# Optimization experiments

Measured on AMD Instinct MI355X. Metric: run time of the kernel, lower is better.

The kernel has to match this reference:

```python
import math
import jax, jax.numpy as jnp
import numpy as np

N = 20000
E = 640000
H = 256          # hidden_channels
HEADS = 8
HD = H // HEADS  # head_dim = 32
RBF = 64
CUT = 5.0
EPS = 1e-5


def setup_inputs() -> dict:
    key = jax.random.key(0)
    ks = jax.random.split(key, 24)
    g = lambda k, shape, scale: (jax.random.normal(k, shape, dtype=jnp.float32) * scale)
    inp = {
        "x": jax.random.normal(ks[0], (N, H), dtype=jnp.float32),
        "vec": jax.random.normal(ks[1], (N, 3, H), dtype=jnp.float32),
        "edge_index": jax.random.randint(ks[2], (2, E), 0, N),
        "r_ij": jax.random.uniform(ks[3], (E,), dtype=jnp.float32) * CUT,
        "f_ij": jax.random.normal(ks[4], (E, RBF), dtype=jnp.float32),
        "d_ij": jax.random.normal(ks[5], (E, 3), dtype=jnp.float32),
        # parameters (weights stored as [in, out], applied as x @ W + b)
        "ln_w": jnp.ones((H,), jnp.float32),
        "ln_b": jnp.zeros((H,), jnp.float32),
        "Wq": g(ks[6], (H, H), 1.0 / math.sqrt(H)),
        "bq": jnp.zeros((H,), jnp.float32),
        "Wk": g(ks[7], (H, H), 1.0 / math.sqrt(H)),
        "bk": jnp.zeros((H,), jnp.float32),
        "Wv": g(ks[8], (H, 3 * H), 1.0 / math.sqrt(H)),
        "bv": jnp.zeros((3 * H,), jnp.float32),
        "Wo": g(ks[9], (H, 3 * H), 1.0 / math.sqrt(H)),
        "bo": jnp.zeros((3 * H,), jnp.float32),
        "Wvec": g(ks[10], (H, 3 * H), 1.0 / math.sqrt(H)),  # no bias
        "Wdk": g(ks[11], (RBF, H), 1.0 / math.sqrt(RBF)),
        "bdk": jnp.zeros((H,), jnp.float32),
        "Wdv": g(ks[12], (RBF, 3 * H), 1.0 / math.sqrt(RBF)),
        "bdv": jnp.zeros((3 * H,), jnp.float32),
    }
    return inp


def reference(x, vec, edge_index, r_ij, f_ij, d_ij,
              ln_w, ln_b, Wq, bq, Wk, bk, Wv, bv, Wo, bo,
              Wvec, Wdk, bdk, Wdv, bdv):
    silu = jax.nn.silu
    n = x.shape[0]

    # LayerNorm over hidden dim
    mu = x.mean(-1, keepdims=True)
    var = ((x - mu) ** 2).mean(-1, keepdims=True)
    xn = (x - mu) / jnp.sqrt(var + EPS) * ln_w + ln_b

    q = (xn @ Wq + bq).reshape(n, HEADS, HD)
    k = (xn @ Wk + bk).reshape(n, HEADS, HD)
    v = (xn @ Wv + bv).reshape(n, HEADS, 3 * HD)

    # vec_proj: [N,3,H] @ [H,3H] -> split into three [N,3,H]
    vec1, vec2, vec3 = jnp.split(vec @ Wvec, 3, axis=-1)
    vec_dot = (vec1 * vec2).sum(axis=1)              # [N, H]
    vec_h = vec.reshape(n, 3, HEADS, HD)

    dk = silu(f_ij @ Wdk + bdk).reshape(-1, HEADS, HD)        # [E,h,hd]
    dv = silu(f_ij @ Wdv + bdv).reshape(-1, HEADS, 3 * HD)    # [E,h,3hd]

    src = edge_index[0]  # j (source)
    dst = edge_index[1]  # i (target), aggregation index

    # per-edge attention with cosine cutoff (cutoff_lower = 0)
    attn = (q[dst] * k[src] * dk).sum(-1)                      # [E, h]
    cut = 0.5 * (jnp.cos(r_ij * (math.pi / CUT)) + 1.0)
    cut = cut * (r_ij < CUT).astype(cut.dtype)
    attn = silu(attn) * cut[:, None]

    v_j = v[src] * dv                                          # [E,h,3hd]
    xm, v1m, v2m = jnp.split(v_j, 3, axis=2)                   # each [E,h,hd]
    xm = xm * attn[..., None]                                  # [E,h,hd]
    # [E,3,h,hd]
    vecm = vec_h[src] * v1m[:, None] + v2m[:, None] * d_ij[:, :, None, None]

    x_agg = jax.ops.segment_sum(xm, dst, num_segments=n).reshape(n, H)
    vec_agg = jax.ops.segment_sum(vecm, dst, num_segments=n).reshape(n, 3, H)

    o1, o2, o3 = jnp.split(x_agg @ Wo + bo, 3, axis=1)
    dx = vec_dot * o2 + o3
    dvec = vec3 * o1[:, None] + vec_agg
    return dx, dvec
```

## Files before the change

### kernel.cpp

```cpp
#include <hip/hip_runtime.h>

#define NN 20000
#define EE 640000
#define H 256
#define H3 768

typedef __attribute__((ext_vector_type(8))) short bfrag;
typedef __attribute__((ext_vector_type(4))) float f32x4;
typedef __attribute__((ext_vector_type(2))) unsigned short u16x2;
typedef __attribute__((ext_vector_type(4))) unsigned short u16x4;
typedef unsigned short u16;

__device__ __forceinline__ float silu_f(float x){ return x / (1.f + __expf(-x)); }

__device__ __forceinline__ u16 f2bf(float f){
  union { float fv; unsigned u; } a; a.fv = f;
  unsigned r = a.u + 0x7fffu + ((a.u >> 16) & 1u);
  return (u16)(r >> 16);
}
__device__ __forceinline__ float bf2f(u16 u){
  union { unsigned u32; float f; } a; a.u32 = ((unsigned)u) << 16; return a.f;
}

__global__ __launch_bounds__(256) void ln_kernel(
    const float* __restrict__ x, const float* __restrict__ w,
    const float* __restrict__ b, u16* __restrict__ xnh, u16* __restrict__ xnl)
{
  int n = blockIdx.x, t = threadIdx.x;
  float v = x[(size_t)n*H + t];
  float s1 = v, s2 = v*v;
  #pragma unroll
  for(int o=32;o>0;o>>=1){ s1 += __shfl_down(s1,o,64); s2 += __shfl_down(s2,o,64); }
  __shared__ float r1[4], r2[4];
  if((t&63)==0){ r1[t>>6]=s1; r2[t>>6]=s2; }
  __syncthreads();
  float mu  = (r1[0]+r1[1]+r1[2]+r1[3]) * (1.f/256.f);
  float ex2 = (r2[0]+r2[1]+r2[2]+r2[3]) * (1.f/256.f);
  float inv = rsqrtf(ex2 - mu*mu + 1e-5f);
  float y = (v - mu)*inv*w[t] + b[t];
  u16 h = f2bf(y);
  xnh[(size_t)n*H + t] = h;
  xnl[(size_t)n*H + t] = f2bf(y - bf2f(h));
}

__device__ __forceinline__ void wconv_body(
    const float* __restrict__ W, int ldw,
    u16* __restrict__ oh, u16* __restrict__ ol, int mode, int bidx)
{
  int idx = bidx*256 + threadIdx.x;
  int n = idx >> 8, k = idx & 255;
  int c = n;
  if(mode == 1){
    int y = n >> 7, j = n & 127;
    c = (j < 64) ? (y*64 + j) : (256 + y*64 + (j - 64));
  }
  float f = W[(size_t)k*ldw + c];
  u16 h = f2bf(f);
  oh[idx] = h;
  ol[idx] = f2bf(f - bf2f(h));
}

__device__ __forceinline__ void convdk_body(
    const float* __restrict__ Wdk, short* __restrict__ wdkf, int bidx)
{
  int idx = bidx*256 + threadIdx.x;
  int k = idx >> 8, c = idx & 255;
  int g = c >> 6, rem = c & 63, n15 = rem >> 2, p = rem & 3;
  int half = k >> 5, quad = (k >> 3) & 3, j = k & 7;
  wdkf[(g*4+p)*1024 + half*512 + quad*128 + n15*8 + j] = (short)f2bf(Wdk[k*H + c]);
}

__device__ __forceinline__ void convdv_body(
    const float* __restrict__ Wdv, short* __restrict__ wdvf, int bidx)
{
  int idx = bidx*256 + threadIdx.x;
  int k = idx / 768, c = idx % 768;
  int h = c / 96, jj = c % 96;
  int st = jj >> 5, r32 = jj & 31, n15 = r32 >> 1, p = r32 & 1;
  int sub = h*6 + st*2 + p;
  int half = k >> 5, quad = (k >> 3) & 3, j = k & 7;
  wdvf[sub*1024 + half*512 + quad*128 + n15*8 + j] = (short)f2bf(Wdv[k*H3 + c]);
}

__global__ __launch_bounds__(256) void prep_kernel(
    const float* __restrict__ Wq, const float* __restrict__ Wk,
    const float* __restrict__ Wv, const float* __restrict__ Wo,
    const float* __restrict__ Wvec,
    const float* __restrict__ Wdk, const float* __restrict__ Wdv,
    const float* __restrict__ bk, const float* __restrict__ bv,
    u16* __restrict__ wtq_h, u16* __restrict__ wtq_l,
    u16* __restrict__ wtkv_h, u16* __restrict__ wtkv_l,
    u16* __restrict__ wto_h, u16* __restrict__ wto_l,
    u16* __restrict__ wtp_h, u16* __restrict__ wtp_l,
    u16* __restrict__ wt3_h, u16* __restrict__ wt3_l,
    short* __restrict__ wdkf, short* __restrict__ wdvf,
    float* __restrict__ bkv, int* __restrict__ deg, int* __restrict__ cursor)
{
  int bx = blockIdx.x;
  if(bx < 256){        wconv_body(Wq,       256, wtq_h,          wtq_l,          0, bx); }
  else if(bx < 512){   wconv_body(Wk,       256, wtkv_h,         wtkv_l,         0, bx-256); }
  else if(bx < 1280){  wconv_body(Wv,       768, wtkv_h+65536,   wtkv_l+65536,   0, bx-512); }
  else if(bx < 2048){  wconv_body(Wo,       768, wto_h,          wto_l,          0, bx-1280); }
  else if(bx < 2560){  wconv_body(Wvec,     768, wtp_h,          wtp_l,          1, bx-2048); }
  else if(bx < 2816){  wconv_body(Wvec+512, 768, wt3_h,          wt3_l,          0, bx-2560); }
  else if(bx < 2880){  convdk_body(Wdk, wdkf, bx-2816); }
  else if(bx < 3072){  convdv_body(Wdv, wdvf, bx-2880); }
  else if(bx < 3076){
    int i = (bx-3072)*256 + threadIdx.x;
    bkv[i] = (i < 256) ? bk[i] : bv[i-256];
  } else {
    int i = (bx-3076)*256 + threadIdx.x;
    if(i < NN){ deg[i] = 0; cursor[i] = 0; }
  }
}

__global__ __launch_bounds__(256) void cvt_vec(
    const float* __restrict__ src, u16* __restrict__ hi, u16* __restrict__ lo, int n4)
{
  int i = blockIdx.x*256 + threadIdx.x;
  if(i < n4){
    float4 v = ((const float4*)src)[i];
    u16x4 oh, olo;
    float a[4] = {v.x, v.y, v.z, v.w};
    #pragma unroll
    for(int j=0;j<4;j++){
      u16 h = f2bf(a[j]);
      oh[j]  = h;
      olo[j] = f2bf(a[j] - bf2f(h));
    }
    ((u16x4*)hi)[i] = oh;
    ((u16x4*)lo)[i] = olo;
  }
}

template<int OUT>
__global__ __launch_bounds__(256) void gemm_split(
    const u16* __restrict__ Ah, const u16* __restrict__ Al,
    const u16* __restrict__ Bh, const u16* __restrict__ Bl,
    const float* __restrict__ bias,
    float* __restrict__ Cf, u16* __restrict__ Ch, int ldw, int M)
{
  int tid  = threadIdx.x;
  int wid  = tid >> 6, lane = tid & 63;
  int ln15 = lane & 15, quad = lane >> 4;
  int wr = wid >> 1, wc = wid & 1;
  int m0 = blockIdx.x*128 + wr*64;
  int n0 = blockIdx.y*128 + wc*64;

  int arow[4];
  #pragma unroll
  for(int mi=0;mi<4;mi++){
    int r = m0 + mi*16 + ln15;
    arow[mi] = (r < M) ? r : (M-1);
  }
  int ncol[4];
  #pragma unroll
  for(int ni=0;ni<4;ni++) ncol[ni] = n0 + ni*16 + ln15;

  f32x4 acc[4][4] = {};

  #pragma unroll 2
  for(int ks=0; ks<8; ks++){
    int kb = ks*32 + quad*8;
    bfrag ah[4], al[4], bh[4], bl[4];
    #pragma unroll
    for(int mi=0;mi<4;mi++){
      ah[mi] = *(const bfrag*)(Ah + ((size_t)arow[mi] << 8) + kb);
      al[mi] = *(const bfrag*)(Al + ((size_t)arow[mi] << 8) + kb);
    }
    #pragma unroll
    for(int ni=0;ni<4;ni++){
      bh[ni] = *(const bfrag*)(Bh + ((size_t)ncol[ni] << 8) + kb);
      bl[ni] = *(const bfrag*)(Bl + ((size_t)ncol[ni] << 8) + kb);
    }
    #pragma unroll
    for(int mi=0;mi<4;mi++)
      #pragma unroll
      for(int ni=0;ni<4;ni++){
        acc[mi][ni] = __builtin_amdgcn_mfma_f32_16x16x32_bf16(ah[mi], bh[ni], acc[mi][ni], 0,0,0);
        acc[mi][ni] = __builtin_amdgcn_mfma_f32_16x16x32_bf16(ah[mi], bl[ni], acc[mi][ni], 0,0,0);
        acc[mi][ni] = __builtin_amdgcn_mfma_f32_16x16x32_bf16(al[mi], bh[ni], acc[mi][ni], 0,0,0);
      }
  }

  #pragma unroll
  for(int mi=0;mi<4;mi++){
    #pragma unroll
    for(int ni=0;ni<4;ni++){
      int col = ncol[ni];
      float bs = bias ? bias[col] : 0.f;
      #pragma unroll
      for(int r=0;r<4;r++){
        int row = m0 + mi*16 + quad*4 + r;
        if(row < M){
          float v = acc[mi][ni][r] + bs;
          if(OUT == 0) Cf[(size_t)row*ldw + col] = v;
          else         Ch[(size_t)row*ldw + col] = f2bf(v);
        }
      }
    }
  }
}

__global__ __launch_bounds__(256) void gemm_vecdot(
    const u16* __restrict__ Ah, const u16* __restrict__ Al,
    const u16* __restrict__ Bh, const u16* __restrict__ Bl,
    float* __restrict__ vd)
{
  __shared__ float l1[96][66];
  __shared__ float l2[96][66];
  int tid  = threadIdx.x;
  int wid  = tid >> 6, lane = tid & 63;
  int ln15 = lane & 15, quad = lane >> 4;
  int wr = wid >> 1, wc = wid & 1;
  int m0 = blockIdx.x*96;
  int y  = blockIdx.y;
  int rowb = wr*48;

  int arow[3];
  #pragma unroll
  for(int mi=0;mi<3;mi++) arow[mi] = m0 + rowb + mi*16 + ln15;
  int ncol[4];
  #pragma unroll
  for(int ni=0;ni<4;ni++) ncol[ni] = y*128 + wc*64 + ni*16 + ln15;

  f32x4 acc[3][4] = {};

  #pragma unroll 2
  for(int ks=0; ks<8; ks++){
    int kb = ks*32 + quad*8;
    bfrag ah[3], al[3], bh[4], bl[4];
    #pragma unroll
    for(int mi=0;mi<3;mi++){
      ah[mi] = *(const bfrag*)(Ah + ((size_t)arow[mi] << 8) + kb);
      al[mi] = *(const bfrag*)(Al + ((size_t)arow[mi] << 8) + kb);
    }
    #pragma unroll
    for(int ni=0;ni<4;ni++){
      bh[ni] = *(const bfrag*)(Bh + ((size_t)ncol[ni] << 8) + kb);
      bl[ni] = *(const bfrag*)(Bl + ((size_t)ncol[ni] << 8) + kb);
    }
    #pragma unroll
    for(int mi=0;mi<3;mi++)
      #pragma unroll
      for(int ni=0;ni<4;ni++){
        acc[mi][ni] = __builtin_amdgcn_mfma_f32_16x16x32_bf16(ah[mi], bh[ni], acc[mi][ni], 0,0,0);
        acc[mi][ni] = __builtin_amdgcn_mfma_f32_16x16x32_bf16(ah[mi], bl[ni], acc[mi][ni], 0,0,0);
        acc[mi][ni] = __builtin_amdgcn_mfma_f32_16x16x32_bf16(al[mi], bh[ni], acc[mi][ni], 0,0,0);
      }
  }

  #pragma unroll
  for(int mi=0;mi<3;mi++)
    #pragma unroll
    for(int ni=0;ni<4;ni++)
      #pragma unroll
      for(int r=0;r<4;r++){
        int lr = rowb + mi*16 + quad*4 + r;
        int lc = ni*16 + ln15;
        if(wc == 0) l1[lr][lc] = acc[mi][ni][r];
        else        l2[lr][lc] = acc[mi][ni][r];
      }
  __syncthreads();

  #pragma unroll
  for(int i=0;i<8;i++){
    int id  = i*256 + tid;
    int n_l = id >> 6, c = id & 63;
    float s = 0.f;
    #pragma unroll
    for(int d=0;d<3;d++) s += l1[n_l*3+d][c] * l2[n_l*3+d][c];
    vd[((size_t)(blockIdx.x*32 + n_l) << 8) + y*64 + c] = s;
  }
}

__global__ __launch_bounds__(256) void hist_kernel(const int* __restrict__ ei, int* __restrict__ deg){
  int e = blockIdx.x*256 + threadIdx.x;
  if(e < EE) atomicAdd(&deg[ei[EE + e]], 1);
}

__global__ __launch_bounds__(1024) void scan_kernel(const int* __restrict__ deg, int* __restrict__ offs){
  __shared__ int ps[1024];
  int t = threadIdx.x;
  int base = t*20;
  int s = 0;
  for(int i=0;i<20;i++){ int idx = base+i; if(idx < NN) s += deg[idx]; }
  ps[t] = s; __syncthreads();
  for(int off=1; off<1024; off<<=1){
    int v = (t>=off) ? ps[t-off] : 0;
    __syncthreads();
    ps[t] += v;
    __syncthreads();
  }
  int run = (t==0) ? 0 : ps[t-1];
  for(int i=0;i<20;i++){
    int idx = base+i;
    if(idx <= NN){
      offs[idx] = run;
      if(idx < NN) run += deg[idx];
    }
  }
}

__global__ __launch_bounds__(256) void scatter_kernel(
    const int* __restrict__ ei, const int* __restrict__ offs,
    int* __restrict__ cursor, int* __restrict__ perm)
{
  int e = blockIdx.x*256 + threadIdx.x;
  if(e >= EE) return;
  int d = ei[EE + e];
  int r = atomicAdd(&cursor[d], 1);
  perm[offs[d] + r] = e;
}

__global__ __launch_bounds__(256,4) void edge_kernel(
    const int* __restrict__ ei, const float* __restrict__ rij,
    const float* __restrict__ fij, const float* __restrict__ dij,
    const float* __restrict__ qg, const u16* __restrict__ kvh,
    const u16* __restrict__ vech,
    const short* __restrict__ wdkf, const short* __restrict__ wdvf,
    const float* __restrict__ bdk, const float* __restrict__ bdv,
    const int* __restrict__ offs, const int* __restrict__ perm,
    u16* __restrict__ xaggh, u16* __restrict__ xaggl, float* __restrict__ dvec)
{
  __shared__ float accs_x[4][256];
  __shared__ float accs_v[4][768];
  __shared__ float attn_s[4][16][8];
  __shared__ int   esrc_s[4][16];
  __shared__ float ecut_s[4][16];
  __shared__ float emask_s[4][16];
  __shared__ float edij_s[4][3][16];

  int tid  = threadIdx.x;
  int wv   = tid >> 6, lane = tid & 63;
  int ln15 = lane & 15, quad = lane >> 4;
  int n    = blockIdx.x*4 + wv;
  int rs = offs[n], re = offs[n+1];

  #pragma unroll
  for(int i=0;i<4;i++)  accs_x[wv][i*64 + lane] = 0.f;
  #pragma unroll
  for(int i=0;i<12;i++) accs_v[wv][i*64 + lane] = 0.f;

  float qreg[16], bkreg[16];
  #pragma unroll
  for(int g=0; g<4; g++){
    float4 t = *(const float4*)(qg + (size_t)n*H + g*64 + 4*ln15);
    qreg[g*4+0]=t.x; qreg[g*4+1]=t.y; qreg[g*4+2]=t.z; qreg[g*4+3]=t.w;
    float4 u = *(const float4*)(bdk + g*64 + 4*ln15);
    bkreg[g*4+0]=u.x; bkreg[g*4+1]=u.y; bkreg[g*4+2]=u.z; bkreg[g*4+3]=u.w;
  }

  for(int base = rs; base < re; base += 16){
    int idx = base + ln15;
    bool val = idx < re;
    int e = perm[val ? idx : rs];
    if(quad == 0){
      esrc_s[wv][ln15] = ei[e];
      float r = rij[e];
      float cu = 0.5f*(__cosf(r*0.6283185307f)+1.f);
      cu = (r < 5.f) ? cu : 0.f;
      ecut_s[wv][ln15]  = val ? cu : 0.f;
      emask_s[wv][ln15] = val ? 1.f : 0.f;
      edij_s[wv][0][ln15] = dij[e*3+0];
      edij_s[wv][1][ln15] = dij[e*3+1];
      edij_s[wv][2][ln15] = dij[e*3+2];
    }
    bfrag af0, af1;
    {
      const float* fr = fij + (size_t)e*64 + quad*8;
      float4 fa = *(const float4*)fr;
      float4 fb = *(const float4*)(fr+4);
      float4 fc = *(const float4*)(fr+32);
      float4 fd = *(const float4*)(fr+36);
      af0[0]=(short)f2bf(fa.x); af0[1]=(short)f2bf(fa.y); af0[2]=(short)f2bf(fa.z); af0[3]=(short)f2bf(fa.w);
      af0[4]=(short)f2bf(fb.x); af0[5]=(short)f2bf(fb.y); af0[6]=(short)f2bf(fb.z); af0[7]=(short)f2bf(fb.w);
      af1[0]=(short)f2bf(fc.x); af1[1]=(short)f2bf(fc.y); af1[2]=(short)f2bf(fc.z); af1[3]=(short)f2bf(fc.w);
      af1[4]=(short)f2bf(fd.x); af1[5]=(short)f2bf(fd.y); af1[6]=(short)f2bf(fd.z); af1[7]=(short)f2bf(fd.w);
    }
    int sns[4]; float mk[4];
    #pragma unroll
    for(int r=0;r<4;r++){
      int el = quad*4 + r;
      sns[r] = esrc_s[wv][el];
      mk[r]  = emask_s[wv][el];
    }

    u16x4 kr[4][4];
    #pragma unroll
    for(int g=0;g<4;g++)
      #pragma unroll
      for(int r=0;r<4;r++)
        kr[g][r] = *(const u16x4*)(kvh + ((size_t)sns[r] << 10) + g*64 + 4*ln15);

    #pragma unroll
    for(int g=0;g<4;g++){
      float lgg[4] = {0.f,0.f,0.f,0.f};
      #pragma unroll
      for(int p=0;p<4;p++){
        const short* wp = wdkf + (g*4+p)*1024 + quad*128 + ln15*8;
        bfrag b0 = *(const bfrag*)wp;
        bfrag b1 = *(const bfrag*)(wp + 512);
        f32x4 acc = {0.f,0.f,0.f,0.f};
        acc = __builtin_amdgcn_mfma_f32_16x16x32_bf16(af0, b0, acc, 0,0,0);
        acc = __builtin_amdgcn_mfma_f32_16x16x32_bf16(af1, b1, acc, 0,0,0);
        float bias = bkreg[g*4+p], qv = qreg[g*4+p];
        #pragma unroll
        for(int r=0;r<4;r++){
          float dk = silu_f(acc[r] + bias);
          lgg[r] += dk * qv * bf2f(kr[g][r][p]);
        }
      }
      #pragma unroll
      for(int r=0;r<4;r++){
        lgg[r] += __shfl_xor(lgg[r],1,64);
        lgg[r] += __shfl_xor(lgg[r],2,64);
        lgg[r] += __shfl_xor(lgg[r],4,64);
      }
      if((ln15 & 7) == 0){
        int hh = 2*g + (ln15 >> 3);
        #pragma unroll
        for(int r=0;r<4;r++){
          int el = quad*4 + r;
          attn_s[wv][el][hh] = silu_f(lgg[r]) * ecut_s[wv][el];
        }
      }
    }

    #pragma unroll 1
    for(int h=0;h<8;h++){
      u16x2 vld[3][4], vcl[3][4];
      #pragma unroll
      for(int st=0;st<3;st++)
        #pragma unroll
        for(int r=0;r<4;r++)
          vld[st][r] = *(const u16x2*)(kvh + ((size_t)sns[r] << 10) + 256 + h*96 + st*32 + 2*ln15);
      #pragma unroll
      for(int d=0;d<3;d++)
        #pragma unroll
        for(int r=0;r<4;r++)
          vcl[d][r] = *(const u16x2*)(vech + (size_t)sns[r]*H3 + d*H + h*32 + 2*ln15);
      float bb[6];
      #pragma unroll
      for(int st=0;st<3;st++){
        float2 b2 = *(const float2*)(bdv + h*96 + st*32 + 2*ln15);
        bb[st*2] = b2.x; bb[st*2+1] = b2.y;
      }
      float at[4];
      #pragma unroll
      for(int r=0;r<4;r++) at[r] = attn_s[wv][quad*4+r][h];

      float v1v[2][4], vjv[2][4];
      float xmt[2] = {0.f, 0.f};
      #pragma unroll
      for(int st=0;st<3;st++){
        #pragma unroll
        for(int p=0;p<2;p++){
          const short* wp = wdvf + (h*6+st*2+p)*1024 + quad*128 + ln15*8;
          bfrag b0 = *(const bfrag*)wp;
          bfrag b1 = *(const bfrag*)(wp + 512);
          f32x4 acc = {0.f,0.f,0.f,0.f};
          acc = __builtin_amdgcn_mfma_f32_16x16x32_bf16(af0, b0, acc, 0,0,0);
          acc = __builtin_amdgcn_mfma_f32_16x16x32_bf16(af1, b1, acc, 0,0,0);
          float bias = bb[st*2+p];
          #pragma unroll
          for(int r=0;r<4;r++){
            float dvv = silu_f(acc[r] + bias) * mk[r];
            float vj = bf2f(vld[st][r][p]) * dvv;
            if(st == 0)      xmt[p]    += vj * at[r];
            else if(st == 1) v1v[p][r]  = vj;
            else             vjv[p][r]  = vj;
          }
        }
      }
      #pragma unroll
      for(int p=0;p<2;p++){
        xmt[p] += __shfl_xor(xmt[p],16,64);
        xmt[p] += __shfl_xor(xmt[p],32,64);
      }
      if(quad == 0){
        accs_x[wv][h*32 + 2*ln15 + 0] += xmt[0];
        accs_x[wv][h*32 + 2*ln15 + 1] += xmt[1];
      }
      #pragma unroll
      for(int d=0;d<3;d++){
        float t0 = 0.f, t1 = 0.f;
        #pragma unroll
        for(int r=0;r<4;r++){
          float dj = edij_s[wv][d][quad*4+r];
          t0 += bf2f(vcl[d][r][0]) * v1v[0][r] + dj * vjv[0][r];
          t1 += bf2f(vcl[d][r][1]) * v1v[1][r] + dj * vjv[1][r];
        }
        t0 += __shfl_xor(t0,16,64); t0 += __shfl_xor(t0,32,64);
        t1 += __shfl_xor(t1,16,64); t1 += __shfl_xor(t1,32,64);
        if(quad == 0){
          accs_v[wv][d*H + h*32 + 2*ln15 + 0] += t0;
          accs_v[wv][d*H + h*32 + 2*ln15 + 1] += t1;
        }
      }
    }
  }

  #pragma unroll
  for(int j=0;j<4;j++){
    float v = accs_x[wv][j*64 + lane];
    u16 h = f2bf(v);
    xaggh[(size_t)n*H + j*64 + lane] = h;
    xaggl[(size_t)n*H + j*64 + lane] = f2bf(v - bf2f(h));
  }
  #pragma unroll
  for(int j=0;j<12;j++) dvec[(size_t)n*H3 + j*64 + lane] = accs_v[wv][j*64 + lane];
}

__global__ __launch_bounds__(256) void final_kernel(
    const float* __restrict__ ob, const float* __restrict__ vd,
    const float* __restrict__ vp3, float* __restrict__ out)
{
  int i = blockIdx.x*256 + threadIdx.x;
  int n = i >> 8, c = i & 255;
  float o1 = ob[(size_t)n*H3 + c];
  float o2 = ob[(size_t)n*H3 + 256 + c];
  float o3 = ob[(size_t)n*H3 + 512 + c];
  out[i] = vd[i]*o2 + o3;
  float* dvec = out + (size_t)NN*H;
  #pragma unroll
  for(int d=0;d<3;d++){
    dvec[(size_t)n*H3 + d*H + c] += vp3[(size_t)(3*n+d)*256 + c] * o1;
  }
}

extern "C" void kernel_launch(void* const* d_in, const int* in_sizes, int n_in,
                              void* d_out, int out_size, void* d_ws, size_t ws_size,
                              hipStream_t stream){
  (void)in_sizes; (void)n_in; (void)out_size; (void)ws_size;
  const float* x    = (const float*)d_in[0];
  const float* vec  = (const float*)d_in[1];
  const int*   ei   = (const int*)d_in[2];
  const float* rij  = (const float*)d_in[3];
  const float* fij  = (const float*)d_in[4];
  const float* dij  = (const float*)d_in[5];
  const float* ln_w = (const float*)d_in[6];
  const float* ln_b = (const float*)d_in[7];
  const float* Wq   = (const float*)d_in[8];
  const float* bq   = (const float*)d_in[9];
  const float* Wk   = (const float*)d_in[10];
  const float* bk   = (const float*)d_in[11];
  const float* Wv   = (const float*)d_in[12];
  const float* bv   = (const float*)d_in[13];
  const float* Wo   = (const float*)d_in[14];
  const float* bo   = (const float*)d_in[15];
  const float* Wvec = (const float*)d_in[16];
  const float* Wdk  = (const float*)d_in[17];
  const float* bdk  = (const float*)d_in[18];
  const float* Wdv  = (const float*)d_in[19];
  const float* bdv  = (const float*)d_in[20];
  float* out = (float*)d_out;
  float* ws  = (float*)d_ws;

  float* vd    = ws;
  float* ob    = ws +  5120000;
  float* vp3   = ws + 20480000;
  float* qb    = ws + 35840000;
  u16*   kvh   = (u16*)(ws + 40960000);
  u16*   vech  = (u16*)(ws + 51200000);
  u16*   vecl  = (u16*)(ws + 58880000);
  u16*   xnh   = (u16*)(ws + 66560000);
  u16*   xnl   = (u16*)(ws + 69120000);
  u16*   xaggh = (u16*)(ws + 71680000);
  u16*   xaggl = (u16*)(ws + 74240000);
  u16*   wt    = (u16*)(ws + 76800000);
  float* bkv   = ws + 77522000;
  int*   deg    = (int*)(ws + 77530000);
  int*   offs   = deg + 20032;
  int*   cursor = offs + 20032;
  int*   perm   = cursor + 20032;
  short* wdkf   = (short*)(perm + 640000);
  short* wdvf   = wdkf + 16384;

  u16* wtq_h  = wt;            u16* wtq_l  = wt +   65536;
  u16* wtkv_h = wt +  131072;  u16* wtkv_l = wt +  393216;
  u16* wto_h  = wt +  655360;  u16* wto_l  = wt +  851968;
  u16* wtp_h  = wt + 1048576;  u16* wtp_l  = wt + 1179648;
  u16* wt3_h  = wt + 1310720;  u16* wt3_l  = wt + 1376256;

  float* dvec = out + (size_t)NN*H;

  prep_kernel<<<3155, 256, 0, stream>>>(Wq, Wk, Wv, Wo, Wvec, Wdk, Wdv, bk, bv,
                                        wtq_h, wtq_l, wtkv_h, wtkv_l, wto_h, wto_l,
                                        wtp_h, wtp_l, wt3_h, wt3_l,
                                        wdkf, wdvf, bkv, deg, cursor);

  ln_kernel<<<20000, 256, 0, stream>>>(x, ln_w, ln_b, xnh, xnl);

  gemm_split<0><<<dim3(157,2), 256, 0, stream>>>(xnh, xnl, wtq_h,  wtq_l,  bq,  qb, nullptr, 256,  20000);
  gemm_split<1><<<dim3(157,8), 256, 0, stream>>>(xnh, xnl, wtkv_h, wtkv_l, bkv, nullptr, kvh, 1024, 20000);

  cvt_vec<<<15000, 256, 0, stream>>>(vec, vech, vecl, 3840000);
  gemm_vecdot<<<dim3(625,4), 256, 0, stream>>>(vech, vecl, wtp_h, wtp_l, vd);
  gemm_split<0><<<dim3(469,2), 256, 0, stream>>>(vech, vecl, wt3_h, wt3_l, nullptr, vp3, nullptr, 256, 60000);

  hist_kernel<<<2500, 256, 0, stream>>>(ei, deg);
  scan_kernel<<<1, 1024, 0, stream>>>(deg, offs);
  scatter_kernel<<<2500, 256, 0, stream>>>(ei, offs, cursor, perm);

  edge_kernel<<<5000, 256, 0, stream>>>(ei, rij, fij, dij, qb, kvh, vech,
                                        wdkf, wdvf, bdk, bdv, offs, perm,
                                        xaggh, xaggl, dvec);

  gemm_split<0><<<dim3(157,6), 256, 0, stream>>>(xaggh, xaggl, wto_h, wto_l, bo, ob, nullptr, 768, 20000);
  final_kernel<<<20000, 256, 0, stream>>>(ob, vd, vp3, out);
}
```

Before: 2.319 ms.

## Split V into planar buffers, prefold vec*v1, pre-convert f_ij, source-sort edge order

The V projection now writes three separate bf16 planes (v0, v1, v2) instead of one interleaved K/V buffer. A new fold kernel precomputes vec*v1 per node, so the edge kernel gathers the folded product and no longer loads v1 separately. f_ij is converted to bf16 once up front, which halves the edge kernel's read of that large tensor. Edges are now sorted by source within each destination bucket (a source CSR followed by an ordered scatter) to improve gather locality. The cost is extra passes, one more buffer write, a serial-ish 64-block scatter, and bf16 rounding of the vec*v1 product, which may reduce accuracy.

```diff
diff --git a/kernel.cpp b/kernel.cpp
--- a/kernel.cpp
+++ b/kernel.cpp
@@ -53,6 +53,9 @@
   if(mode == 1){
     int y = n >> 7, j = n & 127;
     c = (j < 64) ? (y*64 + j) : (256 + y*64 + (j - 64));
+  } else if(mode == 2){
+    int st = n >> 8, rem = n & 255, h = rem >> 5, cc = rem & 31;
+    c = h*96 + st*32 + cc;
   }
   float f = W[(size_t)k*ldw + c];
   u16 h = f2bf(f);
@@ -87,30 +90,45 @@
     const float* __restrict__ Wv, const float* __restrict__ Wo,
     const float* __restrict__ Wvec,
     const float* __restrict__ Wdk, const float* __restrict__ Wdv,
-    const float* __restrict__ bk, const float* __restrict__ bv,
+    const float* __restrict__ bv,
     u16* __restrict__ wtq_h, u16* __restrict__ wtq_l,
-    u16* __restrict__ wtkv_h, u16* __restrict__ wtkv_l,
+    u16* __restrict__ wtk_h, u16* __restrict__ wtk_l,
+    u16* __restrict__ wtv_h, u16* __restrict__ wtv_l,
     u16* __restrict__ wto_h, u16* __restrict__ wto_l,
     u16* __restrict__ wtp_h, u16* __restrict__ wtp_l,
     u16* __restrict__ wt3_h, u16* __restrict__ wt3_l,
     short* __restrict__ wdkf, short* __restrict__ wdvf,
-    float* __restrict__ bkv, int* __restrict__ deg, int* __restrict__ cursor)
+    float* __restrict__ bvp,
+    int* __restrict__ degS, int* __restrict__ degD,
+    int* __restrict__ cursorS, int* __restrict__ cursorD)
 {
   int bx = blockIdx.x;
-  if(bx < 256){        wconv_body(Wq,       256, wtq_h,          wtq_l,          0, bx); }
-  else if(bx < 512){   wconv_body(Wk,       256, wtkv_h,         wtkv_l,         0, bx-256); }
-  else if(bx < 1280){  wconv_body(Wv,       768, wtkv_h+65536,   wtkv_l+65536,   0, bx-512); }
-  else if(bx < 2048){  wconv_body(Wo,       768, wto_h,          wto_l,          0, bx-1280); }
-  else if(bx < 2560){  wconv_body(Wvec,     768, wtp_h,          wtp_l,          1, bx-2048); }
-  else if(bx < 2816){  wconv_body(Wvec+512, 768, wt3_h,          wt3_l,          0, bx-2560); }
+  if(bx < 256){        wconv_body(Wq,       256, wtq_h, wtq_l, 0, bx); }
+  else if(bx < 512){   wconv_body(Wk,       256, wtk_h, wtk_l, 0, bx-256); }
+  else if(bx < 1280){  wconv_body(Wv,       768, wtv_h, wtv_l, 2, bx-512); }
+  else if(bx < 2048){  wconv_body(Wo,       768, wto_h, wto_l, 0, bx-1280); }
+  else if(bx < 2560){  wconv_body(Wvec,     768, wtp_h, wtp_l, 1, bx-2048); }
+  else if(bx < 2816){  wconv_body(Wvec+512, 768, wt3_h, wt3_l, 0, bx-2560); }
   else if(bx < 2880){  convdk_body(Wdk, wdkf, bx-2816); }
   else if(bx < 3072){  convdv_body(Wdv, wdvf, bx-2880); }
-  else if(bx < 3076){
+  else if(bx < 3075){
     int i = (bx-3072)*256 + threadIdx.x;
-    bkv[i] = (i < 256) ? bk[i] : bv[i-256];
+    int st = i >> 8, rem = i & 255, h = rem >> 5, cc = rem & 31;
+    bvp[i] = bv[h*96 + st*32 + cc];
   } else {
-    int i = (bx-3076)*256 + threadIdx.x;
-    if(i < NN){ deg[i] = 0; cursor[i] = 0; }
+    int i = (bx-3075)*256 + threadIdx.x;
+    if(i < NN){ degS[i] = 0; degD[i] = 0; cursorS[i] = 0; cursorD[i] = 0; }
+  }
+}
+
+__global__ __launch_bounds__(256) void cvt_bf(
+    const float* __restrict__ src, u16* __restrict__ dst, int n4)
+{
+  int i = blockIdx.x*256 + threadIdx.x;
+  if(i < n4){
+    float4 v = ((const float4*)src)[i];
+    u16x4 o; o[0]=f2bf(v.x); o[1]=f2bf(v.y); o[2]=f2bf(v.z); o[3]=f2bf(v.w);
+    ((u16x4*)dst)[i] = o;
   }
 }
 
@@ -133,12 +151,29 @@
   }
 }
 
+__global__ __launch_bounds__(256) void fold_kernel(
+    const u16* __restrict__ vech, const u16* __restrict__ v1, u16* __restrict__ wfold)
+{
+  int i4 = blockIdx.x*256 + threadIdx.x;
+  if(i4 >= 3840000) return;
+  int idx = i4*4;
+  int c = idx & 255;
+  int nd = idx >> 8;
+  int n = nd/3;
+  u16x4 a = *(const u16x4*)(vech + idx);
+  u16x4 b = *(const u16x4*)(v1 + n*256 + c);
+  u16x4 o;
+  #pragma unroll
+  for(int j=0;j<4;j++) o[j] = f2bf(bf2f(a[j])*bf2f(b[j]));
+  *(u16x4*)(wfold + idx) = o;
+}
+
 template<int OUT>
 __global__ __launch_bounds__(256) void gemm_split(
     const u16* __restrict__ Ah, const u16* __restrict__ Al,
     const u16* __restrict__ Bh, const u16* __restrict__ Bl,
     const float* __restrict__ bias,
-    float* __restrict__ Cf, u16* __restrict__ Ch, int ldw, int M)
+    float* __restrict__ Cf, u16* __restrict__ Ch, long bufstride, int ldw, int M)
 {
   int tid  = threadIdx.x;
   int wid  = tid >> 6, lane = tid & 63;
@@ -194,8 +229,12 @@
         int row = m0 + mi*16 + quad*4 + r;
         if(row < M){
           float v = acc[mi][ni][r] + bs;
-          if(OUT == 0) Cf[(size_t)row*ldw + col] = v;
-          else         Ch[(size_t)row*ldw + col] = f2bf(v);
+          if(OUT == 0)      Cf[(size_t)row*ldw + col] = v;
+          else if(OUT == 1) Ch[(size_t)row*ldw + col] = f2bf(v);
+          else {
+            int buf = col >> 8;
+            Ch[(size_t)buf*bufstride + (size_t)row*256 + (col & 255)] = f2bf(v);
+          }
         }
       }
     }
@@ -274,9 +313,13 @@
   }
 }
 
-__global__ __launch_bounds__(256) void hist_kernel(const int* __restrict__ ei, int* __restrict__ deg){
+__global__ __launch_bounds__(256) void hist2_kernel(
+    const int* __restrict__ ei, int* __restrict__ degS, int* __restrict__ degD){
   int e = blockIdx.x*256 + threadIdx.x;
-  if(e < EE) atomicAdd(&deg[ei[EE + e]], 1);
+  if(e < EE){
+    atomicAdd(&degS[ei[e]], 1);
+    atomicAdd(&degD[ei[EE + e]], 1);
+  }
 }
 
 __global__ __launch_bounds__(1024) void scan_kernel(const int* __restrict__ deg, int* __restrict__ offs){
@@ -302,22 +345,35 @@
   }
 }
 
-__global__ __launch_bounds__(256) void scatter_kernel(
-    const int* __restrict__ ei, const int* __restrict__ offs,
-    int* __restrict__ cursor, int* __restrict__ perm)
+__global__ __launch_bounds__(256) void scatterS_kernel(
+    const int* __restrict__ ei, const int* __restrict__ offsS,
+    int* __restrict__ cursorS, int* __restrict__ permS)
 {
   int e = blockIdx.x*256 + threadIdx.x;
   if(e >= EE) return;
-  int d = ei[EE + e];
-  int r = atomicAdd(&cursor[d], 1);
-  perm[offs[d] + r] = e;
-}
-
-__global__ __launch_bounds__(256,4) void edge_kernel(
+  int s = ei[e];
+  int r = atomicAdd(&cursorS[s], 1);
+  permS[offsS[s] + r] = e;
+}
+
+__global__ __launch_bounds__(256) void scatter_ord_kernel(
+    const int* __restrict__ ei, const int* __restrict__ permS,
+    const int* __restrict__ offsD, int* __restrict__ cursorD, int* __restrict__ permD)
+{
+  for(int i = blockIdx.x*256 + threadIdx.x; i < EE; i += 64*256){
+    int e = permS[i];
+    int d = ei[EE + e];
+    int r = atomicAdd(&cursorD[d], 1);
+    permD[offsD[d] + r] = e;
+  }
+}
+
+__global__ __launch_bounds__(256,3) void edge_kernel(
     const int* __restrict__ ei, const float* __restrict__ rij,
-    const float* __restrict__ fij, const float* __restrict__ dij,
-    const float* __restrict__ qg, const u16* __restrict__ kvh,
-    const u16* __restrict__ vech,
+    const u16* __restrict__ fh, const float* __restrict__ dij,
+    const float* __restrict__ qg, const u16* __restrict__ kh,
+    const u16* __restrict__ v0, const u16* __restrict__ v2,
+    const u16* __restrict__ wfold,
     const short* __restrict__ wdkf, const short* __restrict__ wdvf,
     const float* __restrict__ bdk, const float* __restrict__ bdv,
     const int* __restrict__ offs, const int* __restrict__ perm,
@@ -366,18 +422,9 @@
       edij_s[wv][1][ln15] = dij[e*3+1];
       edij_s[wv][2][ln15] = dij[e*3+2];
     }
-    bfrag af0, af1;
-    {
-      const float* fr = fij + (size_t)e*64 + quad*8;
-      float4 fa = *(const float4*)fr;
-      float4 fb = *(const float4*)(fr+4);
-      float4 fc = *(const float4*)(fr+32);
-      float4 fd = *(const float4*)(fr+36);
-      af0[0]=(short)f2bf(fa.x); af0[1]=(short)f2bf(fa.y); af0[2]=(short)f2bf(fa.z); af0[3]=(short)f2bf(fa.w);
-      af0[4]=(short)f2bf(fb.x); af0[5]=(short)f2bf(fb.y); af0[6]=(short)f2bf(fb.z); af0[7]=(short)f2bf(fb.w);
-      af1[0]=(short)f2bf(fc.x); af1[1]=(short)f2bf(fc.y); af1[2]=(short)f2bf(fc.z); af1[3]=(short)f2bf(fc.w);
-      af1[4]=(short)f2bf(fd.x); af1[5]=(short)f2bf(fd.y); af1[6]=(short)f2bf(fd.z); af1[7]=(short)f2bf(fd.w);
-    }
+    bfrag af0 = *(const bfrag*)(fh + (size_t)e*64 + quad*8);
+    bfrag af1 = *(const bfrag*)(fh + (size_t)e*64 + 32 + quad*8);
+
     int sns[4]; float mk[4];
     #pragma unroll
     for(int r=0;r<4;r++){
@@ -391,7 +438,7 @@
     for(int g=0;g<4;g++)
       #pragma unroll
       for(int r=0;r<4;r++)
-        kr[g][r] = *(const u16x4*)(kvh + ((size_t)sns[r] << 10) + g*64 + 4*ln15);
+        kr[g][r] = *(const u16x4*)(kh + ((size_t)sns[r] << 8) + g*64 + 4*ln15);
 
     #pragma unroll
     for(int g=0;g<4;g++){
@@ -429,17 +476,17 @@
 
     #pragma unroll 1
     for(int h=0;h<8;h++){
-      u16x2 vld[3][4], vcl[3][4];
-      #pragma unroll
-      for(int st=0;st<3;st++)
-        #pragma unroll
-        for(int r=0;r<4;r++)
-          vld[st][r] = *(const u16x2*)(kvh + ((size_t)sns[r] << 10) + 256 + h*96 + st*32 + 2*ln15);
+      u16x2 v0l[4], v2l[4], wcl[3][4];
+      #pragma unroll
+      for(int r=0;r<4;r++){
+        v0l[r] = *(const u16x2*)(v0 + ((size_t)sns[r] << 8) + h*32 + 2*ln15);
+        v2l[r] = *(const u16x2*)(v2 + ((size_t)sns[r] << 8) + h*32 + 2*ln15);
+      }
       #pragma unroll
       for(int d=0;d<3;d++)
         #pragma unroll
         for(int r=0;r<4;r++)
-          vcl[d][r] = *(const u16x2*)(vech + (size_t)sns[r]*H3 + d*H + h*32 + 2*ln15);
+          wcl[d][r] = *(const u16x2*)(wfold + (size_t)sns[r]*H3 + d*H + h*32 + 2*ln15);
       float bb[6];
       #pragma unroll
       for(int st=0;st<3;st++){
@@ -450,7 +497,7 @@
       #pragma unroll
       for(int r=0;r<4;r++) at[r] = attn_s[wv][quad*4+r][h];
 
-      float v1v[2][4], vjv[2][4];
+      float dv1v[2][4], vjv[2][4];
       float xmt[2] = {0.f, 0.f};
       #pragma unroll
       for(int st=0;st<3;st++){
@@ -466,10 +513,9 @@
           #pragma unroll
           for(int r=0;r<4;r++){
             float dvv = silu_f(acc[r] + bias) * mk[r];
-            float vj = bf2f(vld[st][r][p]) * dvv;
-            if(st == 0)      xmt[p]    += vj * at[r];
-            else if(st == 1) v1v[p][r]  = vj;
-            else             vjv[p][r]  = vj;
+            if(st == 0)      xmt[p]    += bf2f(v0l[r][p]) * dvv * at[r];
+            else if(st == 1) dv1v[p][r] = dvv;
+            else             vjv[p][r]  = bf2f(v2l[r][p]) * dvv;
           }
         }
       }
@@ -488,8 +534,8 @@
         #pragma unroll
         for(int r=0;r<4;r++){
           float dj = edij_s[wv][d][quad*4+r];
-          t0 += bf2f(vcl[d][r][0]) * v1v[0][r] + dj * vjv[0][r];
-          t1 += bf2f(vcl[d][r][1]) * v1v[1][r] + dj * vjv[1][r];
+          t0 += bf2f(wcl[d][r][0]) * dv1v[0][r] + dj * vjv[0][r];
+          t1 += bf2f(wcl[d][r][1]) * dv1v[1][r] + dj * vjv[1][r];
         }
         t0 += __shfl_xor(t0,16,64); t0 += __shfl_xor(t0,32,64);
         t1 += __shfl_xor(t1,16,64); t1 += __shfl_xor(t1,32,64);
@@ -558,55 +604,71 @@
   float* ws  = (float*)d_ws;
 
   float* vd    = ws;
-  float* ob    = ws +  5120000;
-  float* vp3   = ws + 20480000;
-  float* qb    = ws + 35840000;
-  u16*   kvh   = (u16*)(ws + 40960000);
-  u16*   vech  = (u16*)(ws + 51200000);
-  u16*   vecl  = (u16*)(ws + 58880000);
-  u16*   xnh   = (u16*)(ws + 66560000);
-  u16*   xnl   = (u16*)(ws + 69120000);
-  u16*   xaggh = (u16*)(ws + 71680000);
-  u16*   xaggl = (u16*)(ws + 74240000);
+  float* vp3   = ws +  5120000;
+  float* qb    = ws + 20480000;
+  u16*   kh    = (u16*)(ws + 25600000);
+  u16*   v0    = (u16*)(ws + 28160000);
+  u16*   v1    = (u16*)(ws + 30720000);
+  u16*   v2    = (u16*)(ws + 33280000);
+  u16*   vech  = (u16*)(ws + 35840000);
+  u16*   vecl  = (u16*)(ws + 43520000);
+  u16*   wfold = vecl;
+  u16*   xnh   = (u16*)(ws + 51200000);
+  u16*   xnl   = (u16*)(ws + 53760000);
+  u16*   xaggh = xnh;
+  u16*   xaggl = xnl;
+  u16*   fhalf = (u16*)(ws + 56320000);
+  float* ob    = ws + 56320000;
   u16*   wt    = (u16*)(ws + 76800000);
-  float* bkv   = ws + 77522000;
-  int*   deg    = (int*)(ws + 77530000);
-  int*   offs   = deg + 20032;
-  int*   cursor = offs + 20032;
-  int*   perm   = cursor + 20032;
-  short* wdkf   = (short*)(perm + 640000);
-  short* wdvf   = wdkf + 16384;
-
-  u16* wtq_h  = wt;            u16* wtq_l  = wt +   65536;
-  u16* wtkv_h = wt +  131072;  u16* wtkv_l = wt +  393216;
-  u16* wto_h  = wt +  655360;  u16* wto_l  = wt +  851968;
-  u16* wtp_h  = wt + 1048576;  u16* wtp_l  = wt + 1179648;
-  u16* wt3_h  = wt + 1310720;  u16* wt3_l  = wt + 1376256;
+  float* bvp   = ws + 77530000;
+  int*   ip    = (int*)(ws + 77532000);
+  int* degS    = ip;
+  int* offsS   = ip + 20032;
+  int* cursorS = ip + 40064;
+  int* degD    = ip + 60096;
+  int* offsD   = ip + 80128;
+  int* cursorD = ip + 100160;
+  int* permS   = ip + 120192;
+  int* permD   = permS + 640000;
+  short* wdkf  = (short*)(permD + 640000);
+  short* wdvf  = wdkf + 16384;
+
+  u16* wtq_h = wt;            u16* wtq_l = wt +   65536;
+  u16* wtk_h = wt +  131072;  u16* wtk_l = wt +  196608;
+  u16* wtv_h = wt +  262144;  u16* wtv_l = wt +  458752;
+  u16* wto_h = wt +  655360;  u16* wto_l = wt +  851968;
+  u16* wtp_h = wt + 1048576;  u16* wtp_l = wt + 1179648;
+  u16* wt3_h = wt + 1310720;  u16* wt3_l = wt + 1376256;
 
   float* dvec = out + (size_t)NN*H;
 
-  prep_kernel<<<3155, 256, 0, stream>>>(Wq, Wk, Wv, Wo, Wvec, Wdk, Wdv, bk, bv,
-                                        wtq_h, wtq_l, wtkv_h, wtkv_l, wto_h, wto_l,
-                                        wtp_h, wtp_l, wt3_h, wt3_l,
-                                        wdkf, wdvf, bkv, deg, cursor);
+  prep_kernel<<<3154, 256, 0, stream>>>(Wq, Wk, Wv, Wo, Wvec, Wdk, Wdv, bv,
+                                        wtq_h, wtq_l, wtk_h, wtk_l, wtv_h, wtv_l,
+                                        wto_h, wto_l, wtp_h, wtp_l, wt3_h, wt3_l,
+                                        wdkf, wdvf, bvp, degS, degD, cursorS, cursorD);
 
   ln_kernel<<<20000, 256, 0, stream>>>(x, ln_w, ln_b, xnh, xnl);
-
-  gemm_split<0><<<dim3(157,2), 256, 0, stream>>>(xnh, xnl, wtq_h,  wtq_l,  bq,  qb, nullptr, 256,  20000);
-  gemm_split<1><<<dim3(157,8), 256, 0, stream>>>(xnh, xnl, wtkv_h, wtkv_l, bkv, nullptr, kvh, 1024, 20000);
+  cvt_bf<<<40000, 256, 0, stream>>>(fij, fhalf, 10240000);
+
+  gemm_split<0><<<dim3(157,2), 256, 0, stream>>>(xnh, xnl, wtq_h, wtq_l, bq,  qb, nullptr, 0, 256, 20000);
+  gemm_split<1><<<dim3(157,2), 256, 0, stream>>>(xnh, xnl, wtk_h, wtk_l, bk,  nullptr, kh, 0, 256, 20000);
+  gemm_split<2><<<dim3(157,6), 256, 0, stream>>>(xnh, xnl, wtv_h, wtv_l, bvp, nullptr, v0, (long)NN*256, 768, 20000);
 
   cvt_vec<<<15000, 256, 0, stream>>>(vec, vech, vecl, 3840000);
   gemm_vecdot<<<dim3(625,4), 256, 0, stream>>>(vech, vecl, wtp_h, wtp_l, vd);
-  gemm_split<0><<<dim3(469,2), 256, 0, stream>>>(vech, vecl, wt3_h, wt3_l, nullptr, vp3, nullptr, 256, 60000);
-
-  hist_kernel<<<2500, 256, 0, stream>>>(ei, deg);
-  scan_kernel<<<1, 1024, 0, stream>>>(deg, offs);
-  scatter_kernel<<<2500, 256, 0, stream>>>(ei, offs, cursor, perm);
-
-  edge_kernel<<<5000, 256, 0, stream>>>(ei, rij, fij, dij, qb, kvh, vech,
-                                        wdkf, wdvf, bdk, bdv, offs, perm,
+  gemm_split<0><<<dim3(469,2), 256, 0, stream>>>(vech, vecl, wt3_h, wt3_l, nullptr, vp3, nullptr, 0, 256, 60000);
+  fold_kernel<<<15000, 256, 0, stream>>>(vech, v1, wfold);
+
+  hist2_kernel<<<2500, 256, 0, stream>>>(ei, degS, degD);
+  scan_kernel<<<1, 1024, 0, stream>>>(degS, offsS);
+  scan_kernel<<<1, 1024, 0, stream>>>(degD, offsD);
+  scatterS_kernel<<<2500, 256, 0, stream>>>(ei, offsS, cursorS, permS);
+  scatter_ord_kernel<<<64, 256, 0, stream>>>(ei, permS, offsD, cursorD, permD);
+
+  edge_kernel<<<5000, 256, 0, stream>>>(ei, rij, fhalf, dij, qb, kh, v0, v2, wfold,
+                                        wdkf, wdvf, bdk, bdv, offsD, permD,
                                         xaggh, xaggl, dvec);
 
-  gemm_split<0><<<dim3(157,6), 256, 0, stream>>>(xaggh, xaggl, wto_h, wto_l, bo, ob, nullptr, 768, 20000);
+  gemm_split<0><<<dim3(157,6), 256, 0, stream>>>(xaggh, xaggl, wto_h, wto_l, bo, ob, nullptr, 0, 768, 20000);
   final_kernel<<<20000, 256, 0, stream>>>(ob, vd, vp3, out);
 }
```

Result: no change. 2.300 ms (-0.8%).
